# Kernel optimization log

Measured on AMD Instinct MI355X. Metric: run time of the kernel, lower is better.

Reference implementation:

```python
import jax, jax.numpy as jnp
import numpy as np


def _dct2(x):
    """DCT-II over last dim, scipy norm=None scaling (matches the torch rfft trick:
    X_k = 2 * sum_n x_n cos(pi*k*(2n+1)/(2N))). Expressed as one batched matmul."""
    N = x.shape[-1]
    n = jnp.arange(N, dtype=x.dtype)
    k = jnp.arange(N, dtype=x.dtype)
    # D[k, n] = 2*cos(pi*k*(2n+1)/(2N))
    D = 2.0 * jnp.cos((np.pi / (2.0 * N)) * k[:, None] * (2.0 * n[None, :] + 1.0))
    return jnp.einsum('kn,bcn->bck', D, x)


def setup_inputs() -> dict:
    key = jax.random.key(0)
    k0, k1, k2 = jax.random.split(key, 3)
    b, c, l = 32, 512, 1024
    x = jax.random.normal(k0, (b, c, l), dtype=jnp.float32)
    # 1x1 Conv1d weights (kernel_size=1, bias=False) stored as [out, in]
    w1 = jax.random.normal(k1, (2 * c, c), dtype=jnp.float32) / np.float32(np.sqrt(c))
    w2 = jax.random.normal(k2, (c, 2 * c), dtype=jnp.float32) / np.float32(np.sqrt(2 * c))
    ln_w = jnp.ones((l,), dtype=jnp.float32)
    ln_b = jnp.zeros((l,), dtype=jnp.float32)
    return {"x": x, "w1": w1, "w2": w2, "ln_w": ln_w, "ln_b": ln_b}


def reference(x, w1, w2, ln_w, ln_b):
    eps = 1e-6
    freq = _dct2(x)                                   # [b, c, l]
    mu = jnp.mean(freq, axis=-1, keepdims=True)
    var = jnp.var(freq, axis=-1, keepdims=True)       # biased, like nn.LayerNorm
    h = (freq - mu) * jax.lax.rsqrt(var + eps) * ln_w + ln_b
    # fc: Conv1d(c->2c, k=1) -> Dropout(eval: identity) -> ReLU -> Conv1d(2c->c) -> Sigmoid
    h = jax.nn.relu(jnp.einsum('oi,bil->bol', w1, h))  # [b, 2c, l]
    gate = jax.nn.sigmoid(jnp.einsum('oi,bil->bol', w2, h))  # [b, c, l]
    return x * gate
```

## Files before the change

kernel.cpp:

```cpp
#include <hip/hip_runtime.h>
#include <hip/hip_bf16.h>
#include <math.h>

typedef short short8 __attribute__((ext_vector_type(8)));
typedef short short4v __attribute__((ext_vector_type(4)));
typedef float f32x4 __attribute__((ext_vector_type(4)));

__device__ __forceinline__ short f2bf(float f) {
  union { float f; unsigned u; } v; v.f = f;
  unsigned r = v.u + 0x7FFFu + ((v.u >> 16) & 1u);
  return (short)(r >> 16);
}
__device__ __forceinline__ float bf2f(short s) {
  union { unsigned u; float f; } v; v.u = ((unsigned)(unsigned short)s) << 16;
  return v.f;
}

__global__ __launch_bounds__(256) void cast_kernel(const float* __restrict__ in,
                                                   short* __restrict__ out, int n4) {
  int i = blockIdx.x * blockDim.x + threadIdx.x;
  if (i < n4) {
    float4 v = ((const float4*)in)[i];
    short4v o;
    o.x = f2bf(v.x); o.y = f2bf(v.y); o.z = f2bf(v.z); o.w = f2bf(v.w);
    ((short4v*)out)[i] = o;
  }
}

__global__ __launch_bounds__(256) void build_D(short* __restrict__ D) {
  int t = blockIdx.x * 256 + threadIdx.x;
  int k = t >> 10, n = t & 1023;
  const float s = 1.5339807878856412e-03f;
  float arg = (s * (float)k) * (float)(2 * n + 1);
  D[t] = f2bf(2.0f * cosf(arg));
}

__global__ __launch_bounds__(256) void ln_stats(const float2* __restrict__ partial,
                                                float2* __restrict__ musd) {
  int n = blockIdx.x * 256 + threadIdx.x;
  float S = 0.f, Q = 0.f;
#pragma unroll
  for (int r = 0; r < 4; ++r) {
    float2 p = partial[(size_t)r * 16384 + n];
    S += p.x; Q += p.y;
  }
  float mu  = S * (1.f / 1024.f);
  float var = Q * (1.f / 1024.f) - mu * mu;
  float2 o; o.x = mu; o.y = rsqrtf(var + 1e-6f);
  musd[n] = o;
}

__global__ __launch_bounds__(256) void ln_apply(short* __restrict__ freqT,
                                                const float2* __restrict__ musd,
                                                const float* __restrict__ lnw,
                                                const float* __restrict__ lnb) {
  int t = blockIdx.x * 256 + threadIdx.x;
  int c8 = t & 63;
  int k  = (t >> 6) & 1023;
  int b  = t >> 16;
  size_t idx = ((size_t)b << 19) + (size_t)k * 512 + (size_t)c8 * 8;
  short8 v = *(const short8*)&freqT[idx];
  float w  = lnw[k];
  float bb = lnb[k];
  const float2* ms = &musd[b * 512 + c8 * 8];
  short8 o;
#pragma unroll
  for (int j = 0; j < 8; ++j) {
    float f = bf2f(v[j]);
    float2 m = ms[j];
    o[j] = f2bf((f - m.x) * m.y * w + bb);
  }
  *(short8*)&freqT[idx] = o;
}

template<int EPI>
__global__ __launch_bounds__(512, 2) void gemm256(
    const short* __restrict__ A, const short* __restrict__ B,
    void* __restrict__ Cout, const short* __restrict__ XB,
    float2* __restrict__ P, int K, int NT, long strideA, long strideB)
{
  __shared__ short As[2][16384];
  __shared__ short Bs[2][16384];
  const int tid = threadIdx.x;
  const int l   = tid & 63;
  const int w   = tid >> 6;
  const int wm  = w >> 2;
  const int wn  = w & 3;
  const int l7  = l & 7;
  const int lr  = l & 15;
  const int lhi = l >> 4;

  const int nwg = gridDim.x, q = nwg >> 3, orig = blockIdx.x;
  const int wgid = (orig & 7) * q + (orig >> 3);
  int bx, by, bz;
  if (EPI == 0)      { bx = wgid & 3; by = wgid >> 2;       bz = 0; }
  else if (EPI == 1) { bx = wgid & 3; by = (wgid >> 2) & 3; bz = wgid >> 4; }
  else               { by = wgid & 3; bx = (wgid >> 2) & 1; bz = wgid >> 3; }

  const long row0 = (long)bx * 256, col0 = (long)by * 256;
  const short* Ab = A + (size_t)bz * strideA + (size_t)row0 * K;
  const short* Bb = B + (size_t)bz * strideB + (size_t)col0 * K;

  const int rowb  = w * 8 + (l >> 3);
  const int colel = (l7 ^ (l >> 3)) * 8;
  const int abase = (wm * 16 + lr) * 64;
  const int bbase = (wn * 16 + lr) * 64;
  const int s0 = ((lhi    ) ^ l7) * 8;
  const int s1 = ((lhi + 4) ^ l7) * 8;

  f32x4 acc[8][4];
#pragma unroll
  for (int i = 0; i < 8; ++i)
#pragma unroll
    for (int j = 0; j < 4; ++j) acc[i][j] = (f32x4){0.f, 0.f, 0.f, 0.f};

#define GLL(SRC, DST) __builtin_amdgcn_global_load_lds(                      \
      (const __attribute__((address_space(1))) void*)(SRC),                  \
      (__attribute__((address_space(3))) void*)(DST), 16, 0, 0)

#define ST_HALF(OPb, OPlds, T, H) do {                                       \
    const size_t ko_ = (size_t)(T) * 64 + colel;                             \
    const short* sb_ = (OPb) + (size_t)((H) * 128 + rowb) * K + ko_;         \
    short* db_ = &OPlds[(T) & 1][(H) * 8192 + w * 512 + l * 8];              \
    GLL(sb_, db_);                                                           \
    GLL(sb_ + (size_t)64 * K, db_ + 4096);                                   \
  } while (0)

#define LD(PTR, OFF) (*(const short8*)&(PTR)[OFF])
#define MFMA(AV, BV, C) __builtin_amdgcn_mfma_f32_16x16x32_bf16(AV, BV, C, 0, 0, 0)
#define QUAD16(MIH, A0, A1, A2, A3, B0, B1, B2, B3)                          \
    __builtin_amdgcn_s_setprio(1);                                           \
    acc[MIH+0][0]=MFMA(A0,B0,acc[MIH+0][0]); acc[MIH+0][1]=MFMA(A0,B1,acc[MIH+0][1]); \
    acc[MIH+0][2]=MFMA(A0,B2,acc[MIH+0][2]); acc[MIH+0][3]=MFMA(A0,B3,acc[MIH+0][3]); \
    acc[MIH+1][0]=MFMA(A1,B0,acc[MIH+1][0]); acc[MIH+1][1]=MFMA(A1,B1,acc[MIH+1][1]); \
    acc[MIH+1][2]=MFMA(A1,B2,acc[MIH+1][2]); acc[MIH+1][3]=MFMA(A1,B3,acc[MIH+1][3]); \
    acc[MIH+2][0]=MFMA(A2,B0,acc[MIH+2][0]); acc[MIH+2][1]=MFMA(A2,B1,acc[MIH+2][1]); \
    acc[MIH+2][2]=MFMA(A2,B2,acc[MIH+2][2]); acc[MIH+2][3]=MFMA(A2,B3,acc[MIH+2][3]); \
    acc[MIH+3][0]=MFMA(A3,B0,acc[MIH+3][0]); acc[MIH+3][1]=MFMA(A3,B1,acc[MIH+3][1]); \
    acc[MIH+3][2]=MFMA(A3,B2,acc[MIH+3][2]); acc[MIH+3][3]=MFMA(A3,B3,acc[MIH+3][3]); \
    __builtin_amdgcn_s_setprio(0);

#define SBAR __builtin_amdgcn_s_barrier()
#define SCHB __builtin_amdgcn_sched_barrier(0)
#define LGKM0 asm volatile("s_waitcnt lgkmcnt(0)" ::: "memory")

  ST_HALF(Bb, Bs, 0, 0); ST_HALF(Bb, Bs, 0, 1);
  ST_HALF(Ab, As, 0, 0); ST_HALF(Ab, As, 0, 1);
  ST_HALF(Bb, Bs, 1, 0); ST_HALF(Bb, Bs, 1, 1);
  ST_HALF(Ab, As, 1, 0);
  asm volatile("s_waitcnt vmcnt(6)" ::: "memory");
  SBAR;

  short8 b00, b01, b10, b11, b20, b21, b30, b31;
  short8 a0, a1, a2, a3;
  int cur = 0;
  for (int kt = 0; kt < NT; ++kt) {
    const short* Ad = As[cur];
    const short* Bd = Bs[cur];

    a0 = LD(Ad, 0 * 2048 + abase + s0);
    a1 = LD(Ad, 1 * 2048 + abase + s0);
    a2 = LD(Ad, 2 * 2048 + abase + s0);
    a3 = LD(Ad, 3 * 2048 + abase + s0);
    b00 = LD(Bd, bbase + s0);          b01 = LD(Bd, bbase + s1);
    b10 = LD(Bd, 4096 + bbase + s0);   b11 = LD(Bd, 4096 + bbase + s1);
    b20 = LD(Bd, 8192 + bbase + s0);
    b30 = LD(Bd, 12288 + bbase + s0);
    if (kt + 1 < NT) ST_HALF(Ab, As, kt + 1, 1);
    SCHB; SBAR;
    LGKM0; SCHB;
    QUAD16(0, a0, a1, a2, a3, b00, b10, b20, b30)
    SCHB; SBAR;

    a0 = LD(Ad, 8192 + 0 * 2048 + abase + s0);
    a1 = LD(Ad, 8192 + 1 * 2048 + abase + s0);
    a2 = LD(Ad, 8192 + 2 * 2048 + abase + s0);
    a3 = LD(Ad, 8192 + 3 * 2048 + abase + s0);
    b21 = LD(Bd, 8192 + bbase + s1);
    b31 = LD(Bd, 12288 + bbase + s1);
    if (kt + 2 < NT) ST_HALF(Bb, Bs, kt + 2, 0);
    SCHB; SBAR;
    LGKM0; SCHB;
    QUAD16(4, a0, a1, a2, a3, b00, b10, b20, b30)
    SCHB; SBAR;

    a0 = LD(Ad, 0 * 2048 + abase + s1);
    a1 = LD(Ad, 1 * 2048 + abase + s1);
    a2 = LD(Ad, 2 * 2048 + abase + s1);
    a3 = LD(Ad, 3 * 2048 + abase + s1);
    if (kt + 2 < NT) ST_HALF(Bb, Bs, kt + 2, 1);
    SCHB; SBAR;
    LGKM0; SCHB;
    QUAD16(0, a0, a1, a2, a3, b01, b11, b21, b31)
    SCHB; SBAR;

    a0 = LD(Ad, 8192 + 0 * 2048 + abase + s1);
    a1 = LD(Ad, 8192 + 1 * 2048 + abase + s1);
    a2 = LD(Ad, 8192 + 2 * 2048 + abase + s1);
    a3 = LD(Ad, 8192 + 3 * 2048 + abase + s1);
    if (kt + 2 < NT) ST_HALF(Ab, As, kt + 2, 0);
    if (kt + 2 < NT)      { asm volatile("s_waitcnt vmcnt(6)" ::: "memory"); }
    else if (kt + 1 < NT) { asm volatile("s_waitcnt vmcnt(0)" ::: "memory"); }
    SCHB; SBAR;
    LGKM0; SCHB;
    QUAD16(4, a0, a1, a2, a3, b01, b11, b21, b31)
    SCHB; SBAR;

    cur ^= 1;
  }

  float sv[4], qv[4];
#pragma unroll
  for (int ni = 0; ni < 4; ++ni) { sv[ni] = 0.f; qv[ni] = 0.f; }

#pragma unroll
  for (int mi = 0; mi < 8; ++mi) {
#pragma unroll
    for (int ni = 0; ni < 4; ++ni) {
#pragma unroll
      for (int j = 0; j < 4; ++j) {
        int r  = (int)row0 + (mi >> 2) * 128 + (mi & 3) * 32 + wm * 16 + lhi * 4 + j;
        int cc = (int)col0 + (ni >> 1) * 128 + (ni & 1) * 64 + wn * 16 + lr;
        float v = acc[mi][ni][j];
        if (EPI == 0) {
          sv[ni] += v; qv[ni] += v * v;
          ((short*)Cout)[((size_t)(cc >> 9) << 19) + (size_t)r * 512 + (cc & 511)] = f2bf(v);
        } else if (EPI == 1) {
          ((short*)Cout)[(size_t)bz * 1048576 + (size_t)r * 1024 + cc] = f2bf(v > 0.f ? v : 0.f);
        } else {
          size_t idx = (size_t)bz * 524288 + (size_t)r * 1024 + cc;
          float g = 1.f / (1.f + __expf(-v));
          ((float*)Cout)[idx] = bf2f(XB[idx]) * g;
        }
      }
    }
  }

  if (EPI == 0) {
    __syncthreads();
    float* redS = (float*)&As[0][0];
    float* redQ = redS + 2048;
    const int contrib = wm * 4 + lhi;
#pragma unroll
    for (int ni = 0; ni < 4; ++ni) {
      int ccl = (ni >> 1) * 128 + (ni & 1) * 64 + wn * 16 + lr;
      redS[ccl * 8 + contrib] = sv[ni];
      redQ[ccl * 8 + contrib] = qv[ni];
    }
    __syncthreads();
    if (tid < 256) {
      float S = 0.f, Q = 0.f;
#pragma unroll
      for (int i = 0; i < 8; ++i) { S += redS[tid * 8 + i]; Q += redQ[tid * 8 + i]; }
      float2 o; o.x = S; o.y = Q;
      P[(size_t)bx * 16384 + col0 + tid] = o;
    }
  }
#undef QUAD16
#undef MFMA
#undef LD
#undef ST_HALF
#undef GLL
#undef SBAR
#undef SCHB
#undef LGKM0
}

extern "C" void kernel_launch(void* const* d_in, const int* in_sizes, int n_in,
                              void* d_out, int out_size, void* d_ws, size_t ws_size,
                              hipStream_t stream) {
  const float* x    = (const float*)d_in[0];
  const float* w1   = (const float*)d_in[1];
  const float* w2   = (const float*)d_in[2];
  const float* ln_w = (const float*)d_in[3];
  const float* ln_b = (const float*)d_in[4];
  float* out = (float*)d_out;

  char* ws = (char*)d_ws;
  short* x_bf   = (short*)(ws);
  short* D_bf   = (short*)(ws + 33554432);
  short* w1_bf  = (short*)(ws + 35651584);
  short* w2_bf  = (short*)(ws + 36700160);
  short* freqT  = (short*)(ws + 37748736);
  short* z1t    = (short*)(ws + 71303168);
  float2* part  = (float2*)(ws + 138412032);
  float2* musd  = (float2*)(ws + 139460608);

  cast_kernel<<<dim3(16384), dim3(256), 0, stream>>>(x,  x_bf,  16777216 / 4);
  cast_kernel<<<dim3(512),   dim3(256), 0, stream>>>(w1, w1_bf, 524288 / 4);
  cast_kernel<<<dim3(512),   dim3(256), 0, stream>>>(w2, w2_bf, 524288 / 4);
  build_D<<<dim3(4096), dim3(256), 0, stream>>>(D_bf);

  gemm256<0><<<dim3(256), dim3(512), 0, stream>>>(
      D_bf, x_bf, (void*)freqT, nullptr, part, 1024, 16, 0, 0);

  ln_stats<<<dim3(64), dim3(256), 0, stream>>>(part, musd);

  ln_apply<<<dim3(8192), dim3(256), 0, stream>>>(freqT, musd, ln_w, ln_b);

  gemm256<1><<<dim3(512), dim3(512), 0, stream>>>(
      freqT, w1_bf, (void*)z1t, nullptr, nullptr, 512, 8, 524288, 0);

  gemm256<2><<<dim3(256), dim3(512), 0, stream>>>(
      w2_bf, z1t, (void*)out, x_bf, nullptr, 1024, 16, 0, 1048576);
}
```

Measured before the change: 169.7 us.

## Exploit DCT even/odd symmetry to halve the DCT GEMM reduction length

Splits the input into even (x[n]+x[N-1-n]) and odd (x[n]-x[N-1-n]) halves and builds separate even-k and odd-k cosine matrices of size 512x512. The DCT GEMM then runs as two batched GEMMs with K=512 instead of one with K=1024, about half the FLOPs. The output rows are interleaved back and the LN partial sums are indexed per parity. The even/odd buffer reuses the z1t workspace region. The extra rounding of the pre-added sums to bf16 adds some approximation error.

```diff
diff --git a/kernel.cpp b/kernel.cpp
--- a/kernel.cpp
+++ b/kernel.cpp
@@ -27,11 +27,31 @@
   }
 }
 
-__global__ __launch_bounds__(256) void build_D(short* __restrict__ D) {
+__global__ __launch_bounds__(256) void prep_eo(const float* __restrict__ x,
+                                               short* __restrict__ eo,
+                                               short* __restrict__ x_bf) {
   int t = blockIdx.x * 256 + threadIdx.x;
-  int k = t >> 10, n = t & 1023;
+  int bc = t >> 7, n0 = (t & 127) * 4;
+  const float* xr = x + (size_t)bc * 1024;
+  float4 f = *(const float4*)(xr + n0);
+  float4 r = *(const float4*)(xr + 1020 - n0);
+  short4v ef, of, xf, xrv;
+  ef.x = f2bf(f.x + r.w); ef.y = f2bf(f.y + r.z); ef.z = f2bf(f.z + r.y); ef.w = f2bf(f.w + r.x);
+  of.x = f2bf(f.x - r.w); of.y = f2bf(f.y - r.z); of.z = f2bf(f.z - r.y); of.w = f2bf(f.w - r.x);
+  xf.x = f2bf(f.x); xf.y = f2bf(f.y); xf.z = f2bf(f.z); xf.w = f2bf(f.w);
+  xrv.x = f2bf(r.x); xrv.y = f2bf(r.y); xrv.z = f2bf(r.z); xrv.w = f2bf(r.w);
+  *(short4v*)&eo[(size_t)bc * 512 + n0] = ef;
+  *(short4v*)&eo[8388608 + (size_t)bc * 512 + n0] = of;
+  *(short4v*)&x_bf[(size_t)bc * 1024 + n0] = xf;
+  *(short4v*)&x_bf[(size_t)bc * 1024 + 1020 - n0] = xrv;
+}
+
+__global__ __launch_bounds__(256) void build_Deo(short* __restrict__ D) {
+  int t = blockIdx.x * 256 + threadIdx.x;
+  int parity = t >> 18, rem = t & 262143;
+  int k2 = rem >> 9, n = rem & 511;
   const float s = 1.5339807878856412e-03f;
-  float arg = (s * (float)k) * (float)(2 * n + 1);
+  float arg = (s * (float)(2 * k2 + parity)) * (float)(2 * n + 1);
   D[t] = f2bf(2.0f * cosf(arg));
 }
 
@@ -93,7 +113,7 @@
   const int nwg = gridDim.x, q = nwg >> 3, orig = blockIdx.x;
   const int wgid = (orig & 7) * q + (orig >> 3);
   int bx, by, bz;
-  if (EPI == 0)      { bx = wgid & 3; by = wgid >> 2;       bz = 0; }
+  if (EPI == 0)      { bx = wgid & 1; bz = (wgid >> 1) & 1; by = wgid >> 2; }
   else if (EPI == 1) { bx = wgid & 3; by = (wgid >> 2) & 3; bz = wgid >> 4; }
   else               { by = wgid & 3; bx = (wgid >> 2) & 1; bz = wgid >> 3; }
 
@@ -224,7 +244,8 @@
         float v = acc[mi][ni][j];
         if (EPI == 0) {
           sv[ni] += v; qv[ni] += v * v;
-          ((short*)Cout)[((size_t)(cc >> 9) << 19) + (size_t)r * 512 + (cc & 511)] = f2bf(v);
+          int rr = r * 2 + bz;
+          ((short*)Cout)[((size_t)(cc >> 9) << 19) + (size_t)rr * 512 + (cc & 511)] = f2bf(v);
         } else if (EPI == 1) {
           ((short*)Cout)[(size_t)bz * 1048576 + (size_t)r * 1024 + cc] = f2bf(v > 0.f ? v : 0.f);
         } else {
@@ -253,7 +274,7 @@
 #pragma unroll
       for (int i = 0; i < 8; ++i) { S += redS[tid * 8 + i]; Q += redQ[tid * 8 + i]; }
       float2 o; o.x = S; o.y = Q;
-      P[(size_t)bx * 16384 + col0 + tid] = o;
+      P[(size_t)(bz * 2 + bx) * 16384 + col0 + tid] = o;
     }
   }
 #undef QUAD16
@@ -278,21 +299,22 @@
 
   char* ws = (char*)d_ws;
   short* x_bf   = (short*)(ws);
-  short* D_bf   = (short*)(ws + 33554432);
-  short* w1_bf  = (short*)(ws + 35651584);
-  short* w2_bf  = (short*)(ws + 36700160);
-  short* freqT  = (short*)(ws + 37748736);
-  short* z1t    = (short*)(ws + 71303168);
-  float2* part  = (float2*)(ws + 138412032);
-  float2* musd  = (float2*)(ws + 139460608);
-
-  cast_kernel<<<dim3(16384), dim3(256), 0, stream>>>(x,  x_bf,  16777216 / 4);
-  cast_kernel<<<dim3(512),   dim3(256), 0, stream>>>(w1, w1_bf, 524288 / 4);
-  cast_kernel<<<dim3(512),   dim3(256), 0, stream>>>(w2, w2_bf, 524288 / 4);
-  build_D<<<dim3(4096), dim3(256), 0, stream>>>(D_bf);
+  short* Deo    = (short*)(ws + 33554432);
+  short* w1_bf  = (short*)(ws + 34603008);
+  short* w2_bf  = (short*)(ws + 35651584);
+  short* freqT  = (short*)(ws + 36700160);
+  short* z1t    = (short*)(ws + 70254592);
+  short* eo     = z1t;
+  float2* part  = (float2*)(ws + 137363456);
+  float2* musd  = (float2*)(ws + 137887744);
+
+  prep_eo<<<dim3(8192), dim3(256), 0, stream>>>(x, eo, x_bf);
+  cast_kernel<<<dim3(512), dim3(256), 0, stream>>>(w1, w1_bf, 524288 / 4);
+  cast_kernel<<<dim3(512), dim3(256), 0, stream>>>(w2, w2_bf, 524288 / 4);
+  build_Deo<<<dim3(2048), dim3(256), 0, stream>>>(Deo);
 
   gemm256<0><<<dim3(256), dim3(512), 0, stream>>>(
-      D_bf, x_bf, (void*)freqT, nullptr, part, 1024, 16, 0, 0);
+      Deo, eo, (void*)freqT, nullptr, part, 512, 8, 262144, 8388608);
 
   ln_stats<<<dim3(64), dim3(256), 0, stream>>>(part, musd);
 
```

After: 163.7 us. 3.6% less time.
